# Performance work log

Measured on AMD Instinct MI355X. Metric: run time of the kernel, lower is better.

The kernel has to match this reference:

```python
import jax, jax.numpy as jnp
import numpy as np

D_MODEL = 1024
D_FF = 2048
N_EXPERTS = 8
TOP_K = 2


def setup_inputs() -> dict:
    key = jax.random.key(0)
    ks = jax.random.split(key, 10)
    s = 0.02
    return {
        "x": jax.random.normal(ks[0], (2, 1024, D_MODEL), dtype=jnp.float32),
        "gate_w": jax.random.normal(ks[1], (N_EXPERTS, D_MODEL), dtype=jnp.float32) * s,
        "gate_b": jnp.zeros((N_EXPERTS,), jnp.float32),
        "Wg": jax.random.normal(ks[2], (N_EXPERTS, D_MODEL, D_FF), dtype=jnp.float32) * s,
        "bg": jnp.zeros((N_EXPERTS, D_FF), jnp.float32),
        "Wu": jax.random.normal(ks[3], (N_EXPERTS, D_MODEL, D_FF), dtype=jnp.float32) * s,
        "bu": jnp.zeros((N_EXPERTS, D_FF), jnp.float32),
        "Wd": jax.random.normal(ks[4], (N_EXPERTS, D_FF, D_MODEL), dtype=jnp.float32) * s,
        "bd": jnp.zeros((N_EXPERTS, D_MODEL), jnp.float32),
    }


def reference(x, gate_w, gate_b, Wg, bg, Wu, bu, Wd, bd):
    b, s, d = x.shape
    xf = x.reshape(-1, d)                       # (T, d)
    T = xf.shape[0]
    # --- router ---
    logits = xf @ gate_w.T + gate_b             # (T, E)
    probs = jax.nn.softmax(logits.astype(jnp.float32), axis=-1)
    # load-balance loss: KL(ideal || mean_probs), reduction='sum'
    expert_probs = probs.mean(axis=0)
    ideal = 1.0 / N_EXPERTS
    balance_loss = jnp.sum(ideal * (jnp.log(ideal) - jnp.log(expert_probs + 1e-9)))
    # top-k routing, renormalized
    vals, idx = jax.lax.top_k(probs, TOP_K)     # (T, K)
    w = vals / vals.sum(axis=-1, keepdims=True)
    # per-token per-expert combine weight (T, E); zero for non-selected experts
    cw = jnp.zeros((T, N_EXPERTS), jnp.float32).at[
        jnp.arange(T)[:, None], idx].add(w)
    # --- experts (SwiGLU MLP), batched over E, masked combine ---
    g = jnp.einsum('td,edf->tef', xf, Wg) + bg[None]   # (T, E, F)
    u = jnp.einsum('td,edf->tef', xf, Wu) + bu[None]
    h = jax.nn.silu(g) * u
    out = jnp.einsum('tef,efd->ted', h, Wd) + bd[None]  # (T, E, d)
    y = jnp.einsum('ted,te->td', out, cw.astype(x.dtype))
    return y.reshape(b, s, d), balance_loss
```

## Files before the change

kernel.cpp:

```cpp
#include <hip/hip_runtime.h>
#include <hip/hip_bf16.h>


#define D_MODEL 1024
#define D_FF    2048
#define N_EXP   8
#define T_TOK   2048
#define MAXTILES 40

typedef __attribute__((ext_vector_type(8))) short bf16x8;
typedef __attribute__((ext_vector_type(8))) ushort u16x8;
typedef __attribute__((ext_vector_type(4))) float f32x4;

__device__ __forceinline__ ushort f2bf(float f) {
    union { float f; unsigned u; } c; c.f = f;
    unsigned u = c.u;
    return (ushort)((u + 0x7fffu + ((u >> 16) & 1u)) >> 16);
}

__device__ __forceinline__ void glds16(const void* g, void* l) {
    __builtin_amdgcn_global_load_lds(
        (const __attribute__((address_space(1))) unsigned int*)g,
        (__attribute__((address_space(3))) unsigned int*)l, 16, 0, 0);
}

__global__ __launch_bounds__(256) void k_prep_w(
    const float* __restrict__ Wg, const float* __restrict__ Wu, const float* __restrict__ Wd,
    ushort* __restrict__ Wgt, ushort* __restrict__ Wut, ushort* __restrict__ Wdt)
{
    __shared__ __align__(16) ushort lds[16384];

    int s = blockIdx.x;
    int which = blockIdx.y;
    int tid = threadIdx.x;
    int e = s >> 7;

    const float* src; ushort* dst;
    int kt, kb, kbp;
    size_t soff;
    if (which == 2) {
        src = Wd; dst = Wdt;
        kt = (s >> 2) & 31; kbp = s & 3; kb = 0;
        soff = (size_t)e * 2048 * 1024 + (size_t)(kt * 64 + kbp * 16) * 1024;
    } else {
        src = which ? Wu : Wg; dst = which ? Wut : Wgt;
        kt = (s >> 3) & 15; kb = s & 7; kbp = 0;
        soff = (size_t)e * 1024 * 2048 + (size_t)(kt * 64 + kb * 8) * 2048;
    }
    const float4* p = (const float4*)(src + soff);

#pragma unroll
    for (int i = 0; i < 16; i++) {
        float4 v = p[i * 256 + tid];
        ushort4 o;
        o.x = f2bf(v.x); o.y = f2bf(v.y); o.z = f2bf(v.z); o.w = f2bf(v.w);
        *(ushort4*)&lds[(i * 256 + tid) * 4] = o;
    }
    __syncthreads();

    u16x8 in[8];
    if (which == 2) {
        int th = tid >> 7, tc = tid & 127;
#pragma unroll
        for (int ko = 0; ko < 8; ko++)
            in[ko] = *(const u16x8*)&lds[(th * 8 + ko) * 1024 + tc * 8];
    } else {
#pragma unroll
        for (int ko = 0; ko < 8; ko++)
            in[ko] = *(const u16x8*)&lds[ko * 2048 + tid * 8];
    }
    u16x8 out[8];
#pragma unroll
    for (int j = 0; j < 8; j++)
#pragma unroll
        for (int ko = 0; ko < 8; ko++)
            out[j][ko] = in[ko][j];
    __syncthreads();

    int swz = (tid & 7) << 4;
#pragma unroll
    for (int j = 0; j < 8; j++)
        *(u16x8*)((char*)lds + ((((8 * tid + j) * 16) ^ swz))) = out[j];
    __syncthreads();

#pragma unroll
    for (int i = 0; i < 8; i++) {
        int c = i * 256 + tid;
        u16x8 v = *(const u16x8*)((char*)lds + ((c * 16) ^ (((c >> 3) & 7) << 4)));
        int R = c >> 7, q = c & 127;
        size_t gaddr;
        if (which == 2) {
            int kb2 = R >> 3, ntp = R & 7;
            gaddr = (size_t)(e * 256 + ntp * 32 + kt) * 8192 + (kbp * 2 + kb2) * 1024 + q * 8;
        } else {
            gaddr = (size_t)(e * 256 + R * 16 + kt) * 8192 + kb * 1024 + q * 8;
        }
        *(u16x8*)&dst[gaddr] = v;
    }
}

__global__ __launch_bounds__(256) void k_router(
    const float* __restrict__ x, const float* __restrict__ gw, const float* __restrict__ gb,
    int* cnt, float* probsum, int* tok, int* slotpk, float* wtok,
    ushort* __restrict__ xb)
{
    __shared__ float gws[N_EXP * D_MODEL];
    __shared__ float ps_s[N_EXP];
    __shared__ int   bc_s[N_EXP];
    __shared__ int   gb_s[N_EXP];
    __shared__ int   a_e[64];
    __shared__ int   a_lp[64];

    int tid = threadIdx.x;
    for (int i = tid; i < N_EXP * D_MODEL / 4; i += 256)
        ((float4*)gws)[i] = ((const float4*)gw)[i];
    if (tid < N_EXP) { ps_s[tid] = 0.f; bc_s[tid] = 0; }
    __syncthreads();

    int wave = tid >> 6, lane = tid & 63;

    for (int it = 0; it < 8; it++) {
        int tb = it * 4 + wave;
        int t = blockIdx.x * 32 + tb;
        const float4* xr = (const float4*)(x + (size_t)t * D_MODEL);
        ushort* xbr = xb + (size_t)t * D_MODEL;

        float acc[N_EXP];
#pragma unroll
        for (int e = 0; e < N_EXP; e++) acc[e] = 0.f;
#pragma unroll
        for (int q = 0; q < 4; q++) {
            int idx = q * 64 + lane;
            float4 xv = xr[idx];
            ushort4 xc;
            xc.x = f2bf(xv.x); xc.y = f2bf(xv.y); xc.z = f2bf(xv.z); xc.w = f2bf(xv.w);
            *(ushort4*)&xbr[idx * 4] = xc;
#pragma unroll
            for (int e = 0; e < N_EXP; e++) {
                float4 gv = ((const float4*)(gws + e * D_MODEL))[idx];
                acc[e] += xv.x * gv.x + xv.y * gv.y + xv.z * gv.z + xv.w * gv.w;
            }
        }
#pragma unroll
        for (int off = 32; off > 0; off >>= 1) {
#pragma unroll
            for (int e = 0; e < N_EXP; e++) acc[e] += __shfl_xor(acc[e], off, 64);
        }
        if (lane == 0) {
            float l[N_EXP], m = -1e30f;
#pragma unroll
            for (int e = 0; e < N_EXP; e++) { l[e] = acc[e] + gb[e]; m = fmaxf(m, l[e]); }
            float p[N_EXP], s = 0.f;
#pragma unroll
            for (int e = 0; e < N_EXP; e++) { p[e] = expf(l[e] - m); s += p[e]; }
            float inv = 1.f / s;
#pragma unroll
            for (int e = 0; e < N_EXP; e++) { p[e] *= inv; atomicAdd(&ps_s[e], p[e]); }
            int i0 = 0; float v0 = p[0];
#pragma unroll
            for (int e = 1; e < N_EXP; e++) if (p[e] > v0) { v0 = p[e]; i0 = e; }
            int i1 = -1; float v1 = -1.f;
#pragma unroll
            for (int e = 0; e < N_EXP; e++) if (e != i0 && p[e] > v1) { v1 = p[e]; i1 = e; }
            float winv = 1.f / (v0 + v1);
            int lp0 = atomicAdd(&bc_s[i0], 1);
            int lp1 = atomicAdd(&bc_s[i1], 1);
            a_e[tb * 2 + 0] = i0; a_lp[tb * 2 + 0] = lp0;
            a_e[tb * 2 + 1] = i1; a_lp[tb * 2 + 1] = lp1;
            wtok[t * 2 + 0] = v0 * winv;
            wtok[t * 2 + 1] = v1 * winv;
        }
    }
    __syncthreads();
    if (tid < N_EXP) {
        gb_s[tid] = atomicAdd(&cnt[tid], bc_s[tid]);
        atomicAdd(&probsum[tid], ps_s[tid]);
    }
    __syncthreads();
    if (tid < 64) {
        int tb = tid >> 1, k = tid & 1;
        int t = blockIdx.x * 32 + tb;
        int e = a_e[tid];
        int slot = gb_s[e] + a_lp[tid];
        tok[e * T_TOK + slot] = t;
        slotpk[t * 2 + k] = (e << 16) | slot;
    }
}

__global__ void k_base_loss(const int* __restrict__ cnt, const float* __restrict__ probsum,
                            int* abase, int* tile, float* loss_out)
{
    if (threadIdx.x == 0 && blockIdx.x == 0) {
        int b = 0, nt = 0;
        float loss = 0.f;
        for (int e = 0; e < N_EXP; e++) {
            abase[e] = b;
            for (int m0 = 0; m0 < cnt[e]; m0 += 128)
                tile[nt++] = (e << 16) | m0;
            b += ((cnt[e] + 127) >> 7) * 128;
            float mean = probsum[e] * (1.0f / T_TOK);
            loss += 0.125f * (logf(0.125f) - logf(mean + 1e-9f));
        }
        for (; nt < MAXTILES; nt++) tile[nt] = -1;
        *loss_out = loss;
    }
}

__global__ __launch_bounds__(256, 2) void k_expert_gu(
    const ushort* __restrict__ Wgt, const ushort* __restrict__ Wut,
    const float* __restrict__ bg, const float* __restrict__ bu,
    const ushort* __restrict__ xb, const int* __restrict__ cnt,
    const int* __restrict__ abase, const int* __restrict__ tile,
    const int* __restrict__ tok, ushort* __restrict__ h_t)
{
    int ti = tile[blockIdx.x];
    if (ti < 0) return;
    int e = ti >> 16, m0 = ti & 0xffff;
    int ne = cnt[e];
    int nt = blockIdx.y;
    int n0 = nt * 128;
    int stile = (abase[e] >> 7) + (m0 >> 7);

    __shared__ __align__(16) ushort As[128 * 88];
    __shared__ __align__(16) ushort Bg_s[8192];
    __shared__ __align__(16) ushort Bu_s[8192];

    int tid = threadIdx.x;
    int lane = tid & 63, wave = tid >> 6;
    int wm = (wave & 1) * 64, wn = (wave >> 1) * 64;

    int arow = tid >> 1;
    int akh = (tid & 1) * 32;
    int atok = tok[e * T_TOK + min(m0 + arow, ne - 1)];
    const ushort* xrow = xb + (size_t)atok * D_MODEL;

    const char* gbase = (const char*)(Wgt + (size_t)(e * 16 + nt) * 16 * 8192);
    const char* ubase = (const char*)(Wut + (size_t)(e * 16 + nt) * 16 * 8192);
    int goff = tid * 16;
    int loff = (tid >> 6) * 1024;

    f32x4 accg[4][4], accu[4][4];
#pragma unroll
    for (int i = 0; i < 4; i++)
#pragma unroll
        for (int j = 0; j < 4; j++) {
            accg[i][j] = (f32x4){0.f, 0.f, 0.f, 0.f};
            accu[i][j] = (f32x4){0.f, 0.f, 0.f, 0.f};
        }

    for (int kt = 0; kt < D_MODEL / 64; kt++) {
        __syncthreads();
#pragma unroll
        for (int q = 0; q < 4; q++)
            *(uint4*)&As[arow * 88 + akh + q * 8] = *(const uint4*)&xrow[kt * 64 + akh + q * 8];
        const char* gsrc = gbase + kt * 16384;
        const char* usrc = ubase + kt * 16384;
#pragma unroll
        for (int q = 0; q < 4; q++) {
            glds16(gsrc + q * 4096 + goff, (char*)Bg_s + q * 4096 + loff);
            glds16(usrc + q * 4096 + goff, (char*)Bu_s + q * 4096 + loff);
        }
        __syncthreads();
#pragma unroll
        for (int ks = 0; ks < 2; ks++) {
            bf16x8 af[4];
            int arow_f = wm + (lane & 15);
            int akb = ks * 32 + (lane >> 4) * 8;
#pragma unroll
            for (int sm = 0; sm < 4; sm++)
                af[sm] = *(const bf16x8*)&As[(arow_f + sm * 16) * 88 + akb];
            int bkb = ks * 4 + (lane >> 4);
#pragma unroll
            for (int sn = 0; sn < 4; sn++) {
                int ncol = wn + sn * 16 + (lane & 15);
                bf16x8 bgf = *(const bf16x8*)&Bg_s[(bkb * 128 + ncol) * 8];
                bf16x8 buf = *(const bf16x8*)&Bu_s[(bkb * 128 + ncol) * 8];
#pragma unroll
                for (int sm = 0; sm < 4; sm++) {
                    accg[sm][sn] = __builtin_amdgcn_mfma_f32_16x16x32_bf16(af[sm], bgf, accg[sm][sn], 0, 0, 0);
                    accu[sm][sn] = __builtin_amdgcn_mfma_f32_16x16x32_bf16(af[sm], buf, accu[sm][sn], 0, 0, 0);
                }
            }
        }
    }
    int rbase = wm + ((lane >> 4) << 2);
    int cbase = wn + (lane & 15);
    size_t tbase = (size_t)stile * 32 * 8192;
#pragma unroll
    for (int sm = 0; sm < 4; sm++) {
#pragma unroll
        for (int r = 0; r < 4; r++) {
            int pos = m0 + rbase + sm * 16 + r;
            if (pos < ne) {
                int row = pos & 127;
#pragma unroll
                for (int sn = 0; sn < 4; sn++) {
                    int col = n0 + cbase + sn * 16;
                    float g = accg[sm][sn][r] + bg[e * D_FF + col];
                    float u = accu[sm][sn][r] + bu[e * D_FF + col];
                    float hv = (g / (1.f + expf(-g))) * u;
                    int ktb = col >> 6, kb = (col >> 3) & 7, ko = col & 7;
                    h_t[tbase + (size_t)ktb * 8192 + (kb * 128 + row) * 8 + ko] = f2bf(hv);
                }
            }
        }
    }
}

__global__ __launch_bounds__(256, 2) void k_expert_down(
    const ushort* __restrict__ Wdt, const float* __restrict__ bd,
    const ushort* __restrict__ h_t, const int* __restrict__ cnt,
    const int* __restrict__ abase, const int* __restrict__ tile,
    float* __restrict__ outp)
{
    int ti = tile[blockIdx.x];
    if (ti < 0) return;
    int e = ti >> 16, m0 = ti & 0xffff;
    int ne = cnt[e];
    int nt = blockIdx.y;
    int n0 = nt * 128;
    int stile = (abase[e] >> 7) + (m0 >> 7);

    __shared__ __align__(16) ushort As8[8192];
    __shared__ __align__(16) ushort Bd_s[8192];

    int tid = threadIdx.x;
    int lane = tid & 63, wave = tid >> 6;
    int wm = (wave & 1) * 64, wn = (wave >> 1) * 64;

    const char* hbase = (const char*)(h_t + (size_t)stile * 32 * 8192);
    const char* dbase = (const char*)(Wdt + (size_t)(e * 8 + nt) * 32 * 8192);
    int goff = tid * 16;
    int loff = (tid >> 6) * 1024;

    f32x4 acc[4][4];
#pragma unroll
    for (int i = 0; i < 4; i++)
#pragma unroll
        for (int j = 0; j < 4; j++) acc[i][j] = (f32x4){0.f, 0.f, 0.f, 0.f};

    for (int kt = 0; kt < D_FF / 64; kt++) {
        __syncthreads();
        const char* asrc = hbase + kt * 16384;
        const char* bsrc = dbase + kt * 16384;
#pragma unroll
        for (int q = 0; q < 4; q++) {
            glds16(asrc + q * 4096 + goff, (char*)As8 + q * 4096 + loff);
            glds16(bsrc + q * 4096 + goff, (char*)Bd_s + q * 4096 + loff);
        }
        __syncthreads();
#pragma unroll
        for (int ks = 0; ks < 2; ks++) {
            bf16x8 af[4];
            int kb = ks * 4 + (lane >> 4);
            int arow_f = wm + (lane & 15);
#pragma unroll
            for (int sm = 0; sm < 4; sm++)
                af[sm] = *(const bf16x8*)&As8[(kb * 128 + arow_f + sm * 16) * 8];
#pragma unroll
            for (int sn = 0; sn < 4; sn++) {
                int ncol = wn + sn * 16 + (lane & 15);
                bf16x8 bdf = *(const bf16x8*)&Bd_s[(kb * 128 + ncol) * 8];
#pragma unroll
                for (int sm = 0; sm < 4; sm++)
                    acc[sm][sn] = __builtin_amdgcn_mfma_f32_16x16x32_bf16(af[sm], bdf, acc[sm][sn], 0, 0, 0);
            }
        }
    }
    int rbase = wm + ((lane >> 4) << 2);
    int cbase = wn + (lane & 15);
#pragma unroll
    for (int sm = 0; sm < 4; sm++) {
#pragma unroll
        for (int r = 0; r < 4; r++) {
            int pos = m0 + rbase + sm * 16 + r;
            if (pos < ne) {
                size_t ob = (size_t)(abase[e] + pos) * D_MODEL;
#pragma unroll
                for (int sn = 0; sn < 4; sn++) {
                    int col = n0 + cbase + sn * 16;
                    outp[ob + col] = acc[sm][sn][r] + bd[e * D_MODEL + col];
                }
            }
        }
    }
}

__global__ void k_combine(const float* __restrict__ outp, const int* __restrict__ slotpk,
                          const float* __restrict__ wtok, const int* __restrict__ abase,
                          float* __restrict__ y)
{
    int idx = blockIdx.x * 256 + threadIdx.x;
    int t = idx >> 8, j = idx & 255;
    int sp0 = slotpk[t * 2 + 0], sp1 = slotpk[t * 2 + 1];
    float w0 = wtok[t * 2 + 0], w1 = wtok[t * 2 + 1];
    size_t s0 = (size_t)abase[sp0 >> 16] + (sp0 & 0xffff);
    size_t s1 = (size_t)abase[sp1 >> 16] + (sp1 & 0xffff);
    float4 a = ((const float4*)outp)[s0 * (D_MODEL / 4) + j];
    float4 b = ((const float4*)outp)[s1 * (D_MODEL / 4) + j];
    float4 o;
    o.x = w0 * a.x + w1 * b.x;
    o.y = w0 * a.y + w1 * b.y;
    o.z = w0 * a.z + w1 * b.z;
    o.w = w0 * a.w + w1 * b.w;
    ((float4*)y)[idx] = o;
}

extern "C" void kernel_launch(void* const* d_in, const int* in_sizes, int n_in,
                              void* d_out, int out_size, void* d_ws, size_t ws_size,
                              hipStream_t stream)
{
    const float* x  = (const float*)d_in[0];
    const float* gw = (const float*)d_in[1];
    const float* gb = (const float*)d_in[2];
    const float* Wg = (const float*)d_in[3];
    const float* bg = (const float*)d_in[4];
    const float* Wu = (const float*)d_in[5];
    const float* bu = (const float*)d_in[6];
    const float* Wd = (const float*)d_in[7];
    const float* bd = (const float*)d_in[8];
    float* y = (float*)d_out;
    float* loss_out = y + (size_t)T_TOK * D_MODEL;

    char* ws = (char*)d_ws;
    int*    cnt     = (int*)(ws + 0);
    float*  probsum = (float*)(ws + 128);
    int*    abase   = (int*)(ws + 256);
    int*    tiletab = (int*)(ws + 320);
    int*    slotpk  = (int*)(ws + 512);
    float*  wtok    = (float*)(ws + 16896);
    int*    tok     = (int*)(ws + 33280);
    ushort* xb      = (ushort*)(ws + 131072);
    ushort* Wgt     = (ushort*)(ws + 4325376);
    ushort* Wut     = (ushort*)(ws + 37879808);
    ushort* Wdt     = (ushort*)(ws + 71434240);
    ushort* h_t     = (ushort*)(ws + 104988672);
    float*  outp    = (float*)(ws + 125960192);

    hipMemsetAsync(d_ws, 0, 256, stream);
    k_prep_w<<<dim3(1024, 3), dim3(256), 0, stream>>>(Wg, Wu, Wd, Wgt, Wut, Wdt);
    k_router<<<dim3(64), dim3(256), 0, stream>>>(x, gw, gb, cnt, probsum, tok, slotpk, wtok, xb);
    k_base_loss<<<dim3(1), dim3(64), 0, stream>>>(cnt, probsum, abase, tiletab, loss_out);
    k_expert_gu<<<dim3(MAXTILES, 16), dim3(256), 0, stream>>>(Wgt, Wut, bg, bu, xb, cnt, abase, tiletab, tok, h_t);
    k_expert_down<<<dim3(MAXTILES, 8), dim3(256), 0, stream>>>(Wdt, bd, h_t, cnt, abase, tiletab, outp);
    k_combine<<<dim3(2048), dim3(256), 0, stream>>>(outp, slotpk, wtok, abase, y);
}
```

Measured before the change: 386.9 us.

## Fuse weight conversion into router and gate-up kernels to overlap work

The standalone weight conversion kernel is split up. Wg/Wu bf16 conversion now runs as extra blocks inside the router launch, and Wd conversion runs as extra blocks inside the gate/up GEMM launch. Shared memory is unioned so both roles fit in one launch. This removes a launch and lets the conversion work overlap with the router and the gate/up GEMM. The gate/up GEMM blocks now compete with the Wd conversion blocks for CUs and bandwidth, and the union may raise LDS per block.

```diff
diff --git a/kernel.cpp b/kernel.cpp
--- a/kernel.cpp
+++ b/kernel.cpp
@@ -24,31 +24,15 @@
         (__attribute__((address_space(3))) unsigned int*)l, 16, 0, 0);
 }
 
-__global__ __launch_bounds__(256) void k_prep_w(
-    const float* __restrict__ Wg, const float* __restrict__ Wu, const float* __restrict__ Wd,
-    ushort* __restrict__ Wgt, ushort* __restrict__ Wut, ushort* __restrict__ Wdt)
-{
-    __shared__ __align__(16) ushort lds[16384];
-
-    int s = blockIdx.x;
-    int which = blockIdx.y;
-    int tid = threadIdx.x;
-    int e = s >> 7;
-
-    const float* src; ushort* dst;
-    int kt, kb, kbp;
-    size_t soff;
-    if (which == 2) {
-        src = Wd; dst = Wdt;
-        kt = (s >> 2) & 31; kbp = s & 3; kb = 0;
-        soff = (size_t)e * 2048 * 1024 + (size_t)(kt * 64 + kbp * 16) * 1024;
-    } else {
-        src = which ? Wu : Wg; dst = which ? Wut : Wgt;
-        kt = (s >> 3) & 15; kb = s & 7; kbp = 0;
-        soff = (size_t)e * 1024 * 2048 + (size_t)(kt * 64 + kb * 8) * 2048;
-    }
-    const float4* p = (const float4*)(src + soff);
-
+__device__ __forceinline__ void prep_slab_gwu(
+    int sp, int tid, const float* __restrict__ Wg, const float* __restrict__ Wu,
+    ushort* __restrict__ Wgt, ushort* __restrict__ Wut, ushort* lds)
+{
+    int which = sp >> 10, s = sp & 1023;
+    const float* src = which ? Wu : Wg;
+    ushort* dst = which ? Wut : Wgt;
+    int e = s >> 7, kt = (s >> 3) & 15, kb = s & 7;
+    const float4* p = (const float4*)(src + (size_t)e * 1024 * 2048 + (size_t)(kt * 64 + kb * 8) * 2048);
 #pragma unroll
     for (int i = 0; i < 16; i++) {
         float4 v = p[i * 256 + tid];
@@ -57,18 +41,10 @@
         *(ushort4*)&lds[(i * 256 + tid) * 4] = o;
     }
     __syncthreads();
-
     u16x8 in[8];
-    if (which == 2) {
-        int th = tid >> 7, tc = tid & 127;
-#pragma unroll
-        for (int ko = 0; ko < 8; ko++)
-            in[ko] = *(const u16x8*)&lds[(th * 8 + ko) * 1024 + tc * 8];
-    } else {
-#pragma unroll
-        for (int ko = 0; ko < 8; ko++)
-            in[ko] = *(const u16x8*)&lds[ko * 2048 + tid * 8];
-    }
+#pragma unroll
+    for (int ko = 0; ko < 8; ko++)
+        in[ko] = *(const u16x8*)&lds[ko * 2048 + tid * 8];
     u16x8 out[8];
 #pragma unroll
     for (int j = 0; j < 8; j++)
@@ -76,35 +52,73 @@
         for (int ko = 0; ko < 8; ko++)
             out[j][ko] = in[ko][j];
     __syncthreads();
-
     int swz = (tid & 7) << 4;
 #pragma unroll
     for (int j = 0; j < 8; j++)
-        *(u16x8*)((char*)lds + ((((8 * tid + j) * 16) ^ swz))) = out[j];
-    __syncthreads();
-
+        *(u16x8*)((char*)lds + (((8 * tid + j) * 16) ^ swz)) = out[j];
+    __syncthreads();
 #pragma unroll
     for (int i = 0; i < 8; i++) {
         int c = i * 256 + tid;
         u16x8 v = *(const u16x8*)((char*)lds + ((c * 16) ^ (((c >> 3) & 7) << 4)));
         int R = c >> 7, q = c & 127;
-        size_t gaddr;
-        if (which == 2) {
-            int kb2 = R >> 3, ntp = R & 7;
-            gaddr = (size_t)(e * 256 + ntp * 32 + kt) * 8192 + (kbp * 2 + kb2) * 1024 + q * 8;
-        } else {
-            gaddr = (size_t)(e * 256 + R * 16 + kt) * 8192 + kb * 1024 + q * 8;
-        }
-        *(u16x8*)&dst[gaddr] = v;
-    }
-}
-
-__global__ __launch_bounds__(256) void k_router(
+        *(u16x8*)&dst[(size_t)(e * 256 + R * 16 + kt) * 8192 + kb * 1024 + q * 8] = v;
+    }
+}
+
+__device__ __forceinline__ void prep_slab_wd(
+    int s, int tid, const float* __restrict__ Wd, ushort* __restrict__ Wdt, ushort* lds)
+{
+    int e = s >> 7, kt = (s >> 2) & 31, kbp = s & 3;
+    const float4* p = (const float4*)(Wd + (size_t)e * 2048 * 1024 + (size_t)(kt * 64 + kbp * 16) * 1024);
+#pragma unroll
+    for (int i = 0; i < 16; i++) {
+        float4 v = p[i * 256 + tid];
+        ushort4 o;
+        o.x = f2bf(v.x); o.y = f2bf(v.y); o.z = f2bf(v.z); o.w = f2bf(v.w);
+        *(ushort4*)&lds[(i * 256 + tid) * 4] = o;
+    }
+    __syncthreads();
+    u16x8 in[8];
+    int th = tid >> 7, tc = tid & 127;
+#pragma unroll
+    for (int ko = 0; ko < 8; ko++)
+        in[ko] = *(const u16x8*)&lds[(th * 8 + ko) * 1024 + tc * 8];
+    u16x8 out[8];
+#pragma unroll
+    for (int j = 0; j < 8; j++)
+#pragma unroll
+        for (int ko = 0; ko < 8; ko++)
+            out[j][ko] = in[ko][j];
+    __syncthreads();
+    int swz = (tid & 7) << 4;
+#pragma unroll
+    for (int j = 0; j < 8; j++)
+        *(u16x8*)((char*)lds + (((8 * tid + j) * 16) ^ swz)) = out[j];
+    __syncthreads();
+#pragma unroll
+    for (int i = 0; i < 8; i++) {
+        int c = i * 256 + tid;
+        u16x8 v = *(const u16x8*)((char*)lds + ((c * 16) ^ (((c >> 3) & 7) << 4)));
+        int R = c >> 7, q = c & 127;
+        int kb2 = R >> 3, ntp = R & 7;
+        *(u16x8*)&Wdt[(size_t)(e * 256 + ntp * 32 + kt) * 8192 + (kbp * 2 + kb2) * 1024 + q * 8] = v;
+    }
+}
+
+union SM1 {
+    float gws[N_EXP * D_MODEL];
+    ushort prep[16384];
+};
+
+__global__ __launch_bounds__(256) void k_router_prep(
     const float* __restrict__ x, const float* __restrict__ gw, const float* __restrict__ gb,
     int* cnt, float* probsum, int* tok, int* slotpk, float* wtok,
-    ushort* __restrict__ xb)
-{
-    __shared__ float gws[N_EXP * D_MODEL];
+    ushort* __restrict__ xb,
+    const float* __restrict__ Wg, const float* __restrict__ Wu,
+    ushort* __restrict__ Wgt, ushort* __restrict__ Wut)
+{
+    __shared__ __align__(16) SM1 sm;
     __shared__ float ps_s[N_EXP];
     __shared__ int   bc_s[N_EXP];
     __shared__ int   gb_s[N_EXP];
@@ -112,6 +126,14 @@
     __shared__ int   a_lp[64];
 
     int tid = threadIdx.x;
+    int bid = blockIdx.x;
+
+    if (bid >= 64) {
+        prep_slab_gwu(bid - 64, tid, Wg, Wu, Wgt, Wut, sm.prep);
+        return;
+    }
+
+    float* gws = sm.gws;
     for (int i = tid; i < N_EXP * D_MODEL / 4; i += 256)
         ((float4*)gws)[i] = ((const float4*)gw)[i];
     if (tid < N_EXP) { ps_s[tid] = 0.f; bc_s[tid] = 0; }
@@ -121,7 +143,7 @@
 
     for (int it = 0; it < 8; it++) {
         int tb = it * 4 + wave;
-        int t = blockIdx.x * 32 + tb;
+        int t = bid * 32 + tb;
         const float4* xr = (const float4*)(x + (size_t)t * D_MODEL);
         ushort* xbr = xb + (size_t)t * D_MODEL;
 
@@ -179,7 +201,7 @@
     __syncthreads();
     if (tid < 64) {
         int tb = tid >> 1, k = tid & 1;
-        int t = blockIdx.x * 32 + tb;
+        int t = bid * 32 + tb;
         int e = a_e[tid];
         int slot = gb_s[e] + a_lp[tid];
         tok[e * T_TOK + slot] = t;
@@ -206,12 +228,128 @@
     }
 }
 
-__global__ __launch_bounds__(256, 2) void k_expert_gu(
+struct SM_GU { ushort As[128 * 88]; ushort Bg[8192]; ushort Bu[8192]; };
+union SM3 {
+    SM_GU g;
+    ushort prep[16384];
+};
+
+__global__ __launch_bounds__(256, 2) void k_gu_prepwd(
     const ushort* __restrict__ Wgt, const ushort* __restrict__ Wut,
     const float* __restrict__ bg, const float* __restrict__ bu,
     const ushort* __restrict__ xb, const int* __restrict__ cnt,
     const int* __restrict__ abase, const int* __restrict__ tile,
-    const int* __restrict__ tok, ushort* __restrict__ h_t)
+    const int* __restrict__ tok, ushort* __restrict__ h_t,
+    const float* __restrict__ Wd, ushort* __restrict__ Wdt)
+{
+    __shared__ __align__(16) SM3 sm;
+
+    int bid = blockIdx.x;
+    int tid = threadIdx.x;
+
+    if (bid >= MAXTILES * 16) {
+        prep_slab_wd(bid - MAXTILES * 16, tid, Wd, Wdt, sm.prep);
+        return;
+    }
+
+    int ti = tile[bid % MAXTILES];
+    if (ti < 0) return;
+    int e = ti >> 16, m0 = ti & 0xffff;
+    int ne = cnt[e];
+    int nt = bid / MAXTILES;
+    int n0 = nt * 128;
+    int stile = (abase[e] >> 7) + (m0 >> 7);
+
+    ushort* As = sm.g.As;
+    ushort* Bg_s = sm.g.Bg;
+    ushort* Bu_s = sm.g.Bu;
+
+    int lane = tid & 63, wave = tid >> 6;
+    int wm = (wave & 1) * 64, wn = (wave >> 1) * 64;
+
+    int arow = tid >> 1;
+    int akh = (tid & 1) * 32;
+    int atok = tok[e * T_TOK + min(m0 + arow, ne - 1)];
+    const ushort* xrow = xb + (size_t)atok * D_MODEL;
+
+    const char* gbase = (const char*)(Wgt + (size_t)(e * 16 + nt) * 16 * 8192);
+    const char* ubase = (const char*)(Wut + (size_t)(e * 16 + nt) * 16 * 8192);
+    int goff = tid * 16;
+    int loff = (tid >> 6) * 1024;
+
+    f32x4 accg[4][4], accu[4][4];
+#pragma unroll
+    for (int i = 0; i < 4; i++)
+#pragma unroll
+        for (int j = 0; j < 4; j++) {
+            accg[i][j] = (f32x4){0.f, 0.f, 0.f, 0.f};
+            accu[i][j] = (f32x4){0.f, 0.f, 0.f, 0.f};
+        }
+
+    for (int kt = 0; kt < D_MODEL / 64; kt++) {
+        __syncthreads();
+#pragma unroll
+        for (int q = 0; q < 4; q++)
+            *(uint4*)&As[arow * 88 + akh + q * 8] = *(const uint4*)&xrow[kt * 64 + akh + q * 8];
+        const char* gsrc = gbase + kt * 16384;
+        const char* usrc = ubase + kt * 16384;
+#pragma unroll
+        for (int q = 0; q < 4; q++) {
+            glds16(gsrc + q * 4096 + goff, (char*)Bg_s + q * 4096 + loff);
+            glds16(usrc + q * 4096 + goff, (char*)Bu_s + q * 4096 + loff);
+        }
+        __syncthreads();
+#pragma unroll
+        for (int ks = 0; ks < 2; ks++) {
+            bf16x8 af[4];
+            int arow_f = wm + (lane & 15);
+            int akb = ks * 32 + (lane >> 4) * 8;
+#pragma unroll
+            for (int sm_ = 0; sm_ < 4; sm_++)
+                af[sm_] = *(const bf16x8*)&As[(arow_f + sm_ * 16) * 88 + akb];
+            int bkb = ks * 4 + (lane >> 4);
+#pragma unroll
+            for (int sn = 0; sn < 4; sn++) {
+                int ncol = wn + sn * 16 + (lane & 15);
+                bf16x8 bgf = *(const bf16x8*)&Bg_s[(bkb * 128 + ncol) * 8];
+                bf16x8 buf = *(const bf16x8*)&Bu_s[(bkb * 128 + ncol) * 8];
+#pragma unroll
+                for (int sm_ = 0; sm_ < 4; sm_++) {
+                    accg[sm_][sn] = __builtin_amdgcn_mfma_f32_16x16x32_bf16(af[sm_], bgf, accg[sm_][sn], 0, 0, 0);
+                    accu[sm_][sn] = __builtin_amdgcn_mfma_f32_16x16x32_bf16(af[sm_], buf, accu[sm_][sn], 0, 0, 0);
+                }
+            }
+        }
+    }
+    int rbase = wm + ((lane >> 4) << 2);
+    int cbase = wn + (lane & 15);
+    size_t tbase = (size_t)stile * 32 * 8192;
+#pragma unroll
+    for (int sm_ = 0; sm_ < 4; sm_++) {
+#pragma unroll
+        for (int r = 0; r < 4; r++) {
+            int pos = m0 + rbase + sm_ * 16 + r;
+            if (pos < ne) {
+                int row = pos & 127;
+#pragma unroll
+                for (int sn = 0; sn < 4; sn++) {
+                    int col = n0 + cbase + sn * 16;
+                    float g = accg[sm_][sn][r] + bg[e * D_FF + col];
+                    float u = accu[sm_][sn][r] + bu[e * D_FF + col];
+                    float hv = (g / (1.f + expf(-g))) * u;
+                    int ktb = col >> 6, kb = (col >> 3) & 7, ko = col & 7;
+                    h_t[tbase + (size_t)ktb * 8192 + (kb * 128 + row) * 8 + ko] = f2bf(hv);
+                }
+            }
+        }
+    }
+}
+
+__global__ __launch_bounds__(256, 2) void k_expert_down(
+    const ushort* __restrict__ Wdt, const float* __restrict__ bd,
+    const ushort* __restrict__ h_t, const int* __restrict__ cnt,
+    const int* __restrict__ abase, const int* __restrict__ tile,
+    float* __restrict__ outp)
 {
     int ti = tile[blockIdx.x];
     if (ti < 0) return;
@@ -221,106 +359,6 @@
     int n0 = nt * 128;
     int stile = (abase[e] >> 7) + (m0 >> 7);
 
-    __shared__ __align__(16) ushort As[128 * 88];
-    __shared__ __align__(16) ushort Bg_s[8192];
-    __shared__ __align__(16) ushort Bu_s[8192];
-
-    int tid = threadIdx.x;
-    int lane = tid & 63, wave = tid >> 6;
-    int wm = (wave & 1) * 64, wn = (wave >> 1) * 64;
-
-    int arow = tid >> 1;
-    int akh = (tid & 1) * 32;
-    int atok = tok[e * T_TOK + min(m0 + arow, ne - 1)];
-    const ushort* xrow = xb + (size_t)atok * D_MODEL;
-
-    const char* gbase = (const char*)(Wgt + (size_t)(e * 16 + nt) * 16 * 8192);
-    const char* ubase = (const char*)(Wut + (size_t)(e * 16 + nt) * 16 * 8192);
-    int goff = tid * 16;
-    int loff = (tid >> 6) * 1024;
-
-    f32x4 accg[4][4], accu[4][4];
-#pragma unroll
-    for (int i = 0; i < 4; i++)
-#pragma unroll
-        for (int j = 0; j < 4; j++) {
-            accg[i][j] = (f32x4){0.f, 0.f, 0.f, 0.f};
-            accu[i][j] = (f32x4){0.f, 0.f, 0.f, 0.f};
-        }
-
-    for (int kt = 0; kt < D_MODEL / 64; kt++) {
-        __syncthreads();
-#pragma unroll
-        for (int q = 0; q < 4; q++)
-            *(uint4*)&As[arow * 88 + akh + q * 8] = *(const uint4*)&xrow[kt * 64 + akh + q * 8];
-        const char* gsrc = gbase + kt * 16384;
-        const char* usrc = ubase + kt * 16384;
-#pragma unroll
-        for (int q = 0; q < 4; q++) {
-            glds16(gsrc + q * 4096 + goff, (char*)Bg_s + q * 4096 + loff);
-            glds16(usrc + q * 4096 + goff, (char*)Bu_s + q * 4096 + loff);
-        }
-        __syncthreads();
-#pragma unroll
-        for (int ks = 0; ks < 2; ks++) {
-            bf16x8 af[4];
-            int arow_f = wm + (lane & 15);
-            int akb = ks * 32 + (lane >> 4) * 8;
-#pragma unroll
-            for (int sm = 0; sm < 4; sm++)
-                af[sm] = *(const bf16x8*)&As[(arow_f + sm * 16) * 88 + akb];
-            int bkb = ks * 4 + (lane >> 4);
-#pragma unroll
-            for (int sn = 0; sn < 4; sn++) {
-                int ncol = wn + sn * 16 + (lane & 15);
-                bf16x8 bgf = *(const bf16x8*)&Bg_s[(bkb * 128 + ncol) * 8];
-                bf16x8 buf = *(const bf16x8*)&Bu_s[(bkb * 128 + ncol) * 8];
-#pragma unroll
-                for (int sm = 0; sm < 4; sm++) {
-                    accg[sm][sn] = __builtin_amdgcn_mfma_f32_16x16x32_bf16(af[sm], bgf, accg[sm][sn], 0, 0, 0);
-                    accu[sm][sn] = __builtin_amdgcn_mfma_f32_16x16x32_bf16(af[sm], buf, accu[sm][sn], 0, 0, 0);
-                }
-            }
-        }
-    }
-    int rbase = wm + ((lane >> 4) << 2);
-    int cbase = wn + (lane & 15);
-    size_t tbase = (size_t)stile * 32 * 8192;
-#pragma unroll
-    for (int sm = 0; sm < 4; sm++) {
-#pragma unroll
-        for (int r = 0; r < 4; r++) {
-            int pos = m0 + rbase + sm * 16 + r;
-            if (pos < ne) {
-                int row = pos & 127;
-#pragma unroll
-                for (int sn = 0; sn < 4; sn++) {
-                    int col = n0 + cbase + sn * 16;
-                    float g = accg[sm][sn][r] + bg[e * D_FF + col];
-                    float u = accu[sm][sn][r] + bu[e * D_FF + col];
-                    float hv = (g / (1.f + expf(-g))) * u;
-                    int ktb = col >> 6, kb = (col >> 3) & 7, ko = col & 7;
-                    h_t[tbase + (size_t)ktb * 8192 + (kb * 128 + row) * 8 + ko] = f2bf(hv);
-                }
-            }
-        }
-    }
-}
-
-__global__ __launch_bounds__(256, 2) void k_expert_down(
-    const ushort* __restrict__ Wdt, const float* __restrict__ bd,
-    const ushort* __restrict__ h_t, const int* __restrict__ cnt,
-    const int* __restrict__ abase, const int* __restrict__ tile,
-    float* __restrict__ outp)
-{
-    int ti = tile[blockIdx.x];
-    if (ti < 0) return;
-    int e = ti >> 16, m0 = ti & 0xffff;
-    int ne = cnt[e];
-    int nt = blockIdx.y;
-    int n0 = nt * 128;
-    int stile = (abase[e] >> 7) + (m0 >> 7);
-
     __shared__ __align__(16) ushort As8[8192];
     __shared__ __align__(16) ushort Bd_s[8192];
 
@@ -355,31 +393,31 @@
             int kb = ks * 4 + (lane >> 4);
             int arow_f = wm + (lane & 15);
 #pragma unroll
-            for (int sm = 0; sm < 4; sm++)
-                af[sm] = *(const bf16x8*)&As8[(kb * 128 + arow_f + sm * 16) * 8];
+            for (int sm_ = 0; sm_ < 4; sm_++)
+                af[sm_] = *(const bf16x8*)&As8[(kb * 128 + arow_f + sm_ * 16) * 8];
 #pragma unroll
             for (int sn = 0; sn < 4; sn++) {
                 int ncol = wn + sn * 16 + (lane & 15);
                 bf16x8 bdf = *(const bf16x8*)&Bd_s[(kb * 128 + ncol) * 8];
 #pragma unroll
-                for (int sm = 0; sm < 4; sm++)
-                    acc[sm][sn] = __builtin_amdgcn_mfma_f32_16x16x32_bf16(af[sm], bdf, acc[sm][sn], 0, 0, 0);
+                for (int sm_ = 0; sm_ < 4; sm_++)
+                    acc[sm_][sn] = __builtin_amdgcn_mfma_f32_16x16x32_bf16(af[sm_], bdf, acc[sm_][sn], 0, 0, 0);
             }
         }
     }
     int rbase = wm + ((lane >> 4) << 2);
     int cbase = wn + (lane & 15);
 #pragma unroll
-    for (int sm = 0; sm < 4; sm++) {
+    for (int sm_ = 0; sm_ < 4; sm_++) {
 #pragma unroll
         for (int r = 0; r < 4; r++) {
-            int pos = m0 + rbase + sm * 16 + r;
+            int pos = m0 + rbase + sm_ * 16 + r;
             if (pos < ne) {
                 size_t ob = (size_t)(abase[e] + pos) * D_MODEL;
 #pragma unroll
                 for (int sn = 0; sn < 4; sn++) {
                     int col = n0 + cbase + sn * 16;
-                    outp[ob + col] = acc[sm][sn][r] + bd[e * D_MODEL + col];
+                    outp[ob + col] = acc[sm_][sn][r] + bd[e * D_MODEL + col];
                 }
             }
         }
@@ -437,11 +475,12 @@
     ushort* h_t     = (ushort*)(ws + 104988672);
     float*  outp    = (float*)(ws + 125960192);
 
-    hipMemsetAsync(d_ws, 0, 256, stream);
-    k_prep_w<<<dim3(1024, 3), dim3(256), 0, stream>>>(Wg, Wu, Wd, Wgt, Wut, Wdt);
-    k_router<<<dim3(64), dim3(256), 0, stream>>>(x, gw, gb, cnt, probsum, tok, slotpk, wtok, xb);
+    (void)hipMemsetAsync(d_ws, 0, 256, stream);
+    k_router_prep<<<dim3(64 + 2048), dim3(256), 0, stream>>>(
+        x, gw, gb, cnt, probsum, tok, slotpk, wtok, xb, Wg, Wu, Wgt, Wut);
     k_base_loss<<<dim3(1), dim3(64), 0, stream>>>(cnt, probsum, abase, tiletab, loss_out);
-    k_expert_gu<<<dim3(MAXTILES, 16), dim3(256), 0, stream>>>(Wgt, Wut, bg, bu, xb, cnt, abase, tiletab, tok, h_t);
+    k_gu_prepwd<<<dim3(MAXTILES * 16 + 1024), dim3(256), 0, stream>>>(
+        Wgt, Wut, bg, bu, xb, cnt, abase, tiletab, tok, h_t, Wd, Wdt);
     k_expert_down<<<dim3(MAXTILES, 8), dim3(256), 0, stream>>>(Wdt, bd, h_t, cnt, abase, tiletab, outp);
     k_combine<<<dim3(2048), dim3(256), 0, stream>>>(outp, slotpk, wtok, abase, y);
 }
```

After: 349.0 us. 9.8% less time.
